# Kernel optimization log

Hardware: AMD Instinct MI355X
Metric: run time of the kernel (lower is better)

The kernel has to match this reference:

```python
import jax, jax.numpy as jnp
import numpy as np

DIM = 1024

def setup_inputs() -> dict:
    key = jax.random.key(0)
    ks = jax.random.split(key, 8)
    B, Sx, Sy, D = 4, 2048, 2048, DIM
    s = 1.0 / np.sqrt(D)
    return {
        "x": jax.random.normal(ks[0], (B, Sx, D), jnp.float32),
        "y": jax.random.normal(ks[1], (B, Sy, D), jnp.float32),
        "Wq": jax.random.normal(ks[2], (D, D), jnp.float32) * s,
        "bq": jnp.zeros((D,), jnp.float32),
        "Wk": jax.random.normal(ks[3], (D, D), jnp.float32) * s,
        "bk": jnp.zeros((D,), jnp.float32),
        "Wv": jax.random.normal(ks[4], (D, D), jnp.float32) * s,
        "bv": jnp.zeros((D,), jnp.float32),
    }

def reference(x, y, Wq, bq, Wk, bk, Wv, bv):
    D = x.shape[-1]
    scale = jnp.sqrt(jnp.asarray(D, x.dtype))
    Q = jnp.einsum('bsd,de->bse', x, Wq) + bq  # [B,Sx,D]
    K = jnp.einsum('btd,de->bte', y, Wk) + bk  # [B,Sy,D]
    V = jnp.einsum('btd,de->bte', y, Wv) + bv  # [B,Sy,D]
    scores = jnp.einsum('bse,bte->bst', Q, K) / scale  # [B,Sx,Sy]
    probs = jax.nn.softmax(scores, axis=-1)
    out = jnp.einsum('bst,bte->bse', probs, V)  # [B,Sx,D]
    return out
```

## Files before the change

### kernel.cpp

```cpp
#include <hip/hip_runtime.h>

typedef __bf16 bf16x8_t __attribute__((ext_vector_type(8)));
typedef float f32x16_t __attribute__((ext_vector_type(16)));
typedef unsigned short ushort_t;

__device__ __forceinline__ unsigned short f2bf(float f) {
  unsigned u = __float_as_uint(f);
  u = (u + 0x7FFFu + ((u >> 16) & 1u)) >> 16;
  return (unsigned short)u;
}
__device__ __forceinline__ float bf2f(unsigned short h) {
  return __uint_as_float(((unsigned)h) << 16);
}

__device__ __forceinline__ void gload16(const void* g, void* l) {
  __builtin_amdgcn_global_load_lds(
      (const __attribute__((address_space(1))) unsigned int*)g,
      (__attribute__((address_space(3))) unsigned int*)l, 16, 0, 0);
}

template<int MFR, int EPI, bool OUT_BF16, bool HAS_BIAS>
__global__ __launch_bounds__(256, (MFR == 2 ? 4 : 6))
void gemm32(const ushort_t* __restrict__ A, const ushort_t* __restrict__ A2,
            int nsplit, const ushort_t* __restrict__ Bt,
            void* __restrict__ Cp, const float* __restrict__ bias,
            float* __restrict__ aux,
            int gx, int gy, int K, int lda, int ldb, int ldc,
            long sA, long sB, long sC, float alpha)
{
  constexpr int ATILE = 2048 * MFR;
  constexpr int BUFSZ = ATILE + 4096;
  __shared__ __align__(16) ushort_t sm[2 * BUFSZ];
  const int tid = threadIdx.x;
  const int lane = tid & 63;
  const int w = tid >> 6;
  const int wr = w >> 1, wc = w & 1;

  const int per = gridDim.x >> 3;
  int wg = blockIdx.x;
  wg = (wg & 7) * per + (wg >> 3);
  const int bz = wg / (gx * gy);
  const int rr = wg - bz * gx * gy;
  const int by = rr / gx, bx = rr - by * gx;
  const int bm = by * (64 * MFR), bn = bx * 128;

  const ushort_t* Ab = (bn >= nsplit) ? A2 : A;

  const int rA0 = (w * MFR) * 16 + (lane >> 2);
  const int cswA = (((lane & 3) ^ ((rA0 >> 1) & 3)) << 3);
  const int rB0 = (w * 2) * 16 + (lane >> 2);
  const int cswB = (((lane & 3) ^ ((rB0 >> 1) & 3)) << 3);
  const ushort_t* pA0 = Ab + (long)bz * sA + (long)(bm + rA0) * lda + cswA;
  const ushort_t* pB0 = Bt + (long)bz * sB + (long)(bn + rB0) * ldb + cswB;

  auto stage = [&](int kt, int buf) {
    const int k0 = kt << 5;
    ushort_t* s = sm + buf * BUFSZ;
#pragma unroll
    for (int i = 0; i < MFR; ++i)
      gload16(pA0 + i * 16 * lda + k0, s + (w * MFR + i) * 512);
#pragma unroll
    for (int i = 0; i < 2; ++i)
      gload16(pB0 + i * 16 * ldb + k0, s + ATILE + (w * 2 + i) * 512);
  };

  const int l31 = lane & 31, kh = lane >> 5;
  int offA[MFR][2], offB[2][2];
#pragma unroll
  for (int m = 0; m < MFR; ++m) {
    const int row = wr * (32 * MFR) + m * 32 + l31;
#pragma unroll
    for (int s = 0; s < 2; ++s)
      offA[m][s] = row * 32 + (((s * 2 + kh) ^ ((row >> 1) & 3)) << 3);
  }
#pragma unroll
  for (int n = 0; n < 2; ++n) {
    const int row = wc * 64 + n * 32 + l31;
#pragma unroll
    for (int s = 0; s < 2; ++s)
      offB[n][s] = ATILE + row * 32 + (((s * 2 + kh) ^ ((row >> 1) & 3)) << 3);
  }

  f32x16_t acc[MFR][2];
#pragma unroll
  for (int m = 0; m < MFR; ++m)
#pragma unroll
    for (int n = 0; n < 2; ++n)
#pragma unroll
      for (int i = 0; i < 16; ++i) acc[m][n][i] = 0.f;

  stage(0, 0);
  __syncthreads();

#define LDX(off) __builtin_bit_cast(bf16x8_t, *(const uint4*)(sp + (off)))
  const int nt = K >> 5;
  for (int kt = 0; kt < nt; ++kt) {
    const int cur = kt & 1;
    if (kt + 1 < nt) stage(kt + 1, cur ^ 1);
    const ushort_t* sp = sm + cur * BUFSZ;
    bf16x8_t af[MFR][2], bf[2][2];
#pragma unroll
    for (int m = 0; m < MFR; ++m)
#pragma unroll
      for (int s = 0; s < 2; ++s) af[m][s] = LDX(offA[m][s]);
#pragma unroll
    for (int n = 0; n < 2; ++n)
#pragma unroll
      for (int s = 0; s < 2; ++s) bf[n][s] = LDX(offB[n][s]);
    __builtin_amdgcn_s_setprio(1);
#pragma unroll
    for (int s = 0; s < 2; ++s)
#pragma unroll
      for (int m = 0; m < MFR; ++m)
#pragma unroll
        for (int n = 0; n < 2; ++n)
          acc[m][n] = __builtin_amdgcn_mfma_f32_32x32x16_bf16(
              af[m][s], bf[n][s], acc[m][n], 0, 0, 0);
    __builtin_amdgcn_s_setprio(0);
    __syncthreads();
  }
#undef LDX

  const long zC = (long)bz * sC;
#pragma unroll
  for (int m = 0; m < MFR; ++m) {
    const int growb = bm + wr * (32 * MFR) + m * 32;
    float part[16];
    if constexpr (EPI == 1) {
#pragma unroll
      for (int r = 0; r < 16; ++r) part[r] = 0.f;
    }
#pragma unroll
    for (int n = 0; n < 2; ++n) {
      const int gcol = bn + wc * 64 + n * 32 + l31;
      float bv_ = 0.f;
      if constexpr (HAS_BIAS) bv_ = bias[gcol];
#pragma unroll
      for (int r = 0; r < 16; ++r) {
        const int grow = growb + (r & 3) + 8 * (r >> 2) + 4 * kh;
        float v = acc[m][n][r] * alpha + bv_;
        if constexpr (EPI == 1) {
          const ushort_t pb = f2bf(__expf(v));
          ((ushort_t*)Cp)[zC + (long)grow * ldc + gcol] = pb;
          part[r] += bf2f(pb);
        } else if constexpr (EPI == 2) {
          v *= aux[bz * 2048 + grow];
          ((float*)Cp)[zC + (long)grow * ldc + gcol] = v;
        } else if constexpr (OUT_BF16) {
          ((ushort_t*)Cp)[zC + (long)grow * ldc + gcol] = f2bf(v);
        } else {
          ((float*)Cp)[zC + (long)grow * ldc + gcol] = v;
        }
      }
    }
    if constexpr (EPI == 1) {
#pragma unroll
      for (int step = 1; step < 32; step <<= 1)
#pragma unroll
        for (int r = 0; r < 16; ++r) part[r] += __shfl_xor(part[r], step, 64);
      if (m == 0) {
        __syncthreads();
        float* pf = (float*)sm;
        if (tid < 64 * MFR) pf[tid] = 0.f;
        __syncthreads();
      }
      if (l31 == 0) {
        float* pf = (float*)sm;
#pragma unroll
        for (int r = 0; r < 16; ++r) {
          const int rloc = wr * (32 * MFR) + m * 32 + (r & 3) + 8 * (r >> 2) + 4 * kh;
          atomicAdd(&pf[rloc], part[r]);
        }
      }
    }
  }
  if constexpr (EPI == 1) {
    __syncthreads();
    if (tid < 64 * MFR) {
      const float* pf = (const float*)sm;
      aux[(long)bx * 8192 + bz * 2048 + by * (64 * MFR) + tid] = pf[tid];
    }
  }
}

__global__ __launch_bounds__(256)
void invrow(const float* __restrict__ psumG, float* __restrict__ inv) {
  const int r = blockIdx.x * 256 + threadIdx.x;
  float s = 0.f;
#pragma unroll
  for (int k = 0; k < 16; ++k) s += psumG[(long)k * 8192 + r];
  inv[r] = 1.0f / s;
}

__global__ __launch_bounds__(256)
void conv2(const float* __restrict__ x, const float* __restrict__ y,
           ushort_t* __restrict__ xb, ushort_t* __restrict__ yb) {
  const int b = blockIdx.x;
  const float* in = (b < 4096) ? x : y;
  ushort_t* out = (b < 4096) ? xb : yb;
  const long i = (long)(b & 4095) * 256 + threadIdx.x;
  const float4 a = ((const float4*)in)[i * 2];
  const float4 c = ((const float4*)in)[i * 2 + 1];
  uint4 o;
  o.x = (unsigned)f2bf(a.x) | ((unsigned)f2bf(a.y) << 16);
  o.y = (unsigned)f2bf(a.z) | ((unsigned)f2bf(a.w) << 16);
  o.z = (unsigned)f2bf(c.x) | ((unsigned)f2bf(c.y) << 16);
  o.w = (unsigned)f2bf(c.z) | ((unsigned)f2bf(c.w) << 16);
  ((uint4*)out)[i] = o;
}

__global__ __launch_bounds__(256)
void wtrans3(const float* __restrict__ W0, const float* __restrict__ W1,
             const float* __restrict__ W2, ushort_t* __restrict__ T0,
             ushort_t* __restrict__ T1, ushort_t* __restrict__ T2) {
  const float* W = (blockIdx.z == 0) ? W0 : (blockIdx.z == 1) ? W1 : W2;
  ushort_t* Wt = (blockIdx.z == 0) ? T0 : (blockIdx.z == 1) ? T1 : T2;
  __shared__ float tile[32][33];
  const int bx = blockIdx.x * 32;
  const int by = blockIdx.y * 32;
  const int t = threadIdx.x;
  const int c = t & 31, r0 = t >> 5;
#pragma unroll
  for (int i = 0; i < 4; ++i)
    tile[r0 + i * 8][c] = W[(long)(by + r0 + i * 8) * 1024 + bx + c];
  __syncthreads();
#pragma unroll
  for (int i = 0; i < 4; ++i)
    Wt[(long)(bx + r0 + i * 8) * 1024 + by + c] = f2bf(tile[c][r0 + i * 8]);
}

__global__ __launch_bounds__(256)
void bconcat3(const float* __restrict__ a, const float* __restrict__ b,
              const float* __restrict__ c, float* __restrict__ o) {
  const int i = blockIdx.x * 256 + threadIdx.x;
  o[i] = (i < 1024) ? a[i] : (i < 2048) ? b[i - 1024] : c[i - 2048];
}

__global__ __launch_bounds__(256)
void transpose_bf16(const ushort_t* __restrict__ in, ushort_t* __restrict__ out,
                    int ld_in, int ld_out, long in_bs, long out_bs) {
  __shared__ ushort_t tt[64][65];
  in += (long)blockIdx.z * in_bs;
  out += (long)blockIdx.z * out_bs;
  const int r0 = blockIdx.y * 64, c0 = blockIdx.x * 64;
  const int tc = threadIdx.x & 31;
  const int tr = threadIdx.x >> 5;
#pragma unroll
  for (int i = 0; i < 8; ++i) {
    const unsigned v = *(const unsigned*)(in + (long)(r0 + tr + 8 * i) * ld_in + c0 + tc * 2);
    tt[tr + 8 * i][tc * 2] = (ushort_t)(v & 0xffff);
    tt[tr + 8 * i][tc * 2 + 1] = (ushort_t)(v >> 16);
  }
  __syncthreads();
#pragma unroll
  for (int i = 0; i < 8; ++i) {
    const unsigned v = (unsigned)tt[tc * 2][tr + 8 * i] |
                       ((unsigned)tt[tc * 2 + 1][tr + 8 * i] << 16);
    *(unsigned*)(out + (long)(c0 + tr + 8 * i) * ld_out + r0 + tc * 2) = v;
  }
}

extern "C" void kernel_launch(void* const* d_in, const int* in_sizes, int n_in,
                              void* d_out, int out_size, void* d_ws, size_t ws_size,
                              hipStream_t stream) {
  const float* x  = (const float*)d_in[0];
  const float* y  = (const float*)d_in[1];
  const float* Wq = (const float*)d_in[2];
  const float* bq = (const float*)d_in[3];
  const float* Wk = (const float*)d_in[4];
  const float* bk = (const float*)d_in[5];
  const float* Wv = (const float*)d_in[6];
  const float* bv = (const float*)d_in[7];
  float* out = (float*)d_out;

  const int D = 1024;
  const long MB_ = 1l << 20;

  ushort_t* ws   = (ushort_t*)d_ws;
  ushort_t* Wall = ws;
  ushort_t* QKV8 = ws + 3 * MB_;
  ushort_t* Sb   = ws + 27 * MB_;
  ushort_t* yb   = ws + 27 * MB_;
  ushort_t* xb   = ws + 35 * MB_;
  ushort_t* Vt   = ws + 43 * MB_;
  float*    bias3 = (float*)(ws + 51 * MB_);
  float*    psumG = (float*)(ws + 51 * MB_ + 8192);
  float*    inv   = psumG + 16 * 8192;

  dim3 blk(256);

  conv2<<<dim3(8192), blk, 0, stream>>>(x, y, xb, yb);
  wtrans3<<<dim3(32, 32, 3), blk, 0, stream>>>(
      Wq, Wk, Wv, Wall, Wall + 1 * MB_, Wall + 2 * MB_);
  bconcat3<<<dim3(12), blk, 0, stream>>>(bq, bk, bv, bias3);

  gemm32<2, 0, true, true><<<dim3(1536), blk, 0, stream>>>(
      xb, yb, 1024, Wall, QKV8, bias3, nullptr,
      24, 64, D, D, D, 3072, 0, 0, 0, 1.0f);

  transpose_bf16<<<dim3(16, 32, 4), blk, 0, stream>>>(
      QKV8 + 2048, Vt, 3072, 2048, 2048l * 3072, 1024l * 2048);

  gemm32<1, 1, true, false><<<dim3(2048), blk, 0, stream>>>(
      QKV8, QKV8, 1 << 30, QKV8 + 1024, Sb, nullptr, psumG,
      16, 32, D, 3072, 3072, 2048,
      2048l * 3072, 2048l * 3072, 2048l * 2048, 0.03125f);

  invrow<<<dim3(32), blk, 0, stream>>>(psumG, inv);

  gemm32<1, 2, false, false><<<dim3(1024), blk, 0, stream>>>(
      Sb, Sb, 1 << 30, Vt, out, nullptr, inv,
      8, 32, 2048, 2048, 2048, D,
      2048l * 2048, 1024l * 2048, 2048l * 1024, 1.0f);
}
```

Measured before the change: 236.5 us.

## Use larger 256-row tiles for score and PV GEMMs with new gemm_big kernel

Adds a gemm_big kernel with 256xBN block tiles, where each wave computes a 128x64 sub-tile (4x2 MFMA fragments), and uses it for the QK^T score GEMM (256x256 tiles, 512 threads) and the probs*V GEMM (256x128 tiles). The larger tiles raise arithmetic intensity and cut redundant global and LDS traffic compared with the earlier 64-row and 128-row tiles. The partial row-sum buffer shrinks from 16 to 8 column blocks to match, and gemm32 loses its now-unused epilogue paths. In exchange there are only 256 workgroups, possibly fewer than the number of CUs, and register pressure per thread is higher.

```diff
diff --git a/kernel.cpp b/kernel.cpp
--- a/kernel.cpp
+++ b/kernel.cpp
@@ -17,6 +17,160 @@
   __builtin_amdgcn_global_load_lds(
       (const __attribute__((address_space(1))) unsigned int*)g,
       (__attribute__((address_space(3))) unsigned int*)l, 16, 0, 0);
+}
+
+template<int BN, int EPI>
+__global__ __launch_bounds__((BN / 64) * 128, 2)
+void gemm_big(const ushort_t* __restrict__ A, const ushort_t* __restrict__ Bt,
+              void* __restrict__ Cp, float* __restrict__ aux,
+              int gx, int gy, int K, int lda, int ldb, int ldc,
+              long sA, long sB, long sC, float alpha)
+{
+  constexpr int WC = BN / 64;
+  constexpr int NW = 2 * WC;
+  constexpr int BUFSZ = 8192 + BN * 32;
+  constexpr int A_SPW = 16 / NW;
+  constexpr int B_SPW = (BN / 16) / NW;
+  __shared__ __align__(16) ushort_t sm[2 * BUFSZ];
+
+  const int tid = threadIdx.x;
+  const int lane = tid & 63;
+  const int w = tid >> 6;
+  const int wr = w / WC, wc = w % WC;
+
+  const int per = gridDim.x >> 3;
+  int wg = blockIdx.x;
+  wg = (wg & 7) * per + (wg >> 3);
+  const int bz = wg / (gx * gy);
+  const int rr = wg - bz * gx * gy;
+  const int by = rr / gx, bx = rr - by * gx;
+  const int bm = by * 256, bn = bx * BN;
+
+  const int csw = (((lane & 3) ^ ((lane >> 3) & 3)) << 3);
+  const ushort_t* pA = A + (long)bz * sA +
+      (long)(bm + w * (A_SPW * 16) + (lane >> 2)) * lda + csw;
+  const ushort_t* pB = Bt + (long)bz * sB +
+      (long)(bn + w * (B_SPW * 16) + (lane >> 2)) * ldb + csw;
+
+  auto stage = [&](int kt, int buf) {
+    const int k0 = kt << 5;
+    ushort_t* s = sm + buf * BUFSZ;
+#pragma unroll
+    for (int i = 0; i < A_SPW; ++i)
+      gload16(pA + (long)(i * 16) * lda + k0, s + (w * A_SPW + i) * 512);
+#pragma unroll
+    for (int i = 0; i < B_SPW; ++i)
+      gload16(pB + (long)(i * 16) * ldb + k0, s + 8192 + (w * B_SPW + i) * 512);
+  };
+
+  const int l31 = lane & 31, kh = lane >> 5;
+  const int sw3 = (lane >> 1) & 3;
+  int offA[4][2], offB[2][2];
+#pragma unroll
+  for (int mf = 0; mf < 4; ++mf)
+#pragma unroll
+    for (int ks = 0; ks < 2; ++ks)
+      offA[mf][ks] = (wr * 128 + mf * 32 + l31) * 32 +
+                     (((ks * 2 + kh) ^ sw3) << 3);
+#pragma unroll
+  for (int nf = 0; nf < 2; ++nf)
+#pragma unroll
+    for (int ks = 0; ks < 2; ++ks)
+      offB[nf][ks] = 8192 + (wc * 64 + nf * 32 + l31) * 32 +
+                     (((ks * 2 + kh) ^ sw3) << 3);
+
+  f32x16_t acc[4][2];
+#pragma unroll
+  for (int m = 0; m < 4; ++m)
+#pragma unroll
+    for (int n = 0; n < 2; ++n)
+#pragma unroll
+      for (int i = 0; i < 16; ++i) acc[m][n][i] = 0.f;
+
+  stage(0, 0);
+  __syncthreads();
+
+#define LDX(off) __builtin_bit_cast(bf16x8_t, *(const uint4*)(sp + (off)))
+  const int nt = K >> 5;
+  for (int kt = 0; kt < nt; ++kt) {
+    const int cur = kt & 1;
+    if (kt + 1 < nt) stage(kt + 1, cur ^ 1);
+    const ushort_t* sp = sm + cur * BUFSZ;
+    bf16x8_t af[4][2], bfv[2][2];
+#pragma unroll
+    for (int mf = 0; mf < 4; ++mf)
+#pragma unroll
+      for (int ks = 0; ks < 2; ++ks) af[mf][ks] = LDX(offA[mf][ks]);
+#pragma unroll
+    for (int nf = 0; nf < 2; ++nf)
+#pragma unroll
+      for (int ks = 0; ks < 2; ++ks) bfv[nf][ks] = LDX(offB[nf][ks]);
+    __builtin_amdgcn_s_setprio(1);
+#pragma unroll
+    for (int ks = 0; ks < 2; ++ks)
+#pragma unroll
+      for (int mf = 0; mf < 4; ++mf)
+#pragma unroll
+        for (int nf = 0; nf < 2; ++nf)
+          acc[mf][nf] = __builtin_amdgcn_mfma_f32_32x32x16_bf16(
+              af[mf][ks], bfv[nf][ks], acc[mf][nf], 0, 0, 0);
+    __builtin_amdgcn_s_setprio(0);
+    __syncthreads();
+  }
+#undef LDX
+
+  const long zC = (long)bz * sC;
+  float* pf = (float*)sm;
+  if constexpr (EPI == 1) {
+    if (tid < 256) pf[tid] = 0.f;
+    __syncthreads();
+  }
+#pragma unroll
+  for (int mf = 0; mf < 4; ++mf) {
+    const int growb = bm + wr * 128 + mf * 32;
+    float part[16];
+    if constexpr (EPI == 1) {
+#pragma unroll
+      for (int r = 0; r < 16; ++r) part[r] = 0.f;
+    }
+#pragma unroll
+    for (int nf = 0; nf < 2; ++nf) {
+      const int gcol = bn + wc * 64 + nf * 32 + l31;
+#pragma unroll
+      for (int r = 0; r < 16; ++r) {
+        const int grow = growb + (r & 3) + 8 * (r >> 2) + 4 * kh;
+        float v = acc[mf][nf][r] * alpha;
+        if constexpr (EPI == 1) {
+          const ushort_t pb = f2bf(__expf(v));
+          ((ushort_t*)Cp)[zC + (long)grow * ldc + gcol] = pb;
+          part[r] += bf2f(pb);
+        } else if constexpr (EPI == 2) {
+          v *= aux[bz * 2048 + grow];
+          ((float*)Cp)[zC + (long)grow * ldc + gcol] = v;
+        } else {
+          ((ushort_t*)Cp)[zC + (long)grow * ldc + gcol] = f2bf(v);
+        }
+      }
+    }
+    if constexpr (EPI == 1) {
+#pragma unroll
+      for (int step = 1; step < 32; step <<= 1)
+#pragma unroll
+        for (int r = 0; r < 16; ++r) part[r] += __shfl_xor(part[r], step, 64);
+      if (l31 == 0) {
+#pragma unroll
+        for (int r = 0; r < 16; ++r) {
+          const int rloc = wr * 128 + mf * 32 + (r & 3) + 8 * (r >> 2) + 4 * kh;
+          atomicAdd(&pf[rloc], part[r]);
+        }
+      }
+    }
+  }
+  if constexpr (EPI == 1) {
+    __syncthreads();
+    if (tid < 256)
+      aux[(long)bx * 8192 + bz * 2048 + by * 256 + tid] = pf[tid];
+  }
 }
 
 template<int MFR, int EPI, bool OUT_BF16, bool HAS_BIAS>
@@ -98,7 +252,7 @@
     const int cur = kt & 1;
     if (kt + 1 < nt) stage(kt + 1, cur ^ 1);
     const ushort_t* sp = sm + cur * BUFSZ;
-    bf16x8_t af[MFR][2], bf[2][2];
+    bf16x8_t af[MFR][2], bfv[2][2];
 #pragma unroll
     for (int m = 0; m < MFR; ++m)
 #pragma unroll
@@ -106,7 +260,7 @@
 #pragma unroll
     for (int n = 0; n < 2; ++n)
 #pragma unroll
-      for (int s = 0; s < 2; ++s) bf[n][s] = LDX(offB[n][s]);
+      for (int s = 0; s < 2; ++s) bfv[n][s] = LDX(offB[n][s]);
     __builtin_amdgcn_s_setprio(1);
 #pragma unroll
     for (int s = 0; s < 2; ++s)
@@ -115,7 +269,7 @@
 #pragma unroll
         for (int n = 0; n < 2; ++n)
           acc[m][n] = __builtin_amdgcn_mfma_f32_32x32x16_bf16(
-              af[m][s], bf[n][s], acc[m][n], 0, 0, 0);
+              af[m][s], bfv[n][s], acc[m][n], 0, 0, 0);
     __builtin_amdgcn_s_setprio(0);
     __syncthreads();
   }
@@ -125,11 +279,6 @@
 #pragma unroll
   for (int m = 0; m < MFR; ++m) {
     const int growb = bm + wr * (32 * MFR) + m * 32;
-    float part[16];
-    if constexpr (EPI == 1) {
-#pragma unroll
-      for (int r = 0; r < 16; ++r) part[r] = 0.f;
-    }
 #pragma unroll
     for (int n = 0; n < 2; ++n) {
       const int gcol = bn + wc * 64 + n * 32 + l31;
@@ -138,48 +287,14 @@
 #pragma unroll
       for (int r = 0; r < 16; ++r) {
         const int grow = growb + (r & 3) + 8 * (r >> 2) + 4 * kh;
-        float v = acc[m][n][r] * alpha + bv_;
-        if constexpr (EPI == 1) {
-          const ushort_t pb = f2bf(__expf(v));
-          ((ushort_t*)Cp)[zC + (long)grow * ldc + gcol] = pb;
-          part[r] += bf2f(pb);
-        } else if constexpr (EPI == 2) {
-          v *= aux[bz * 2048 + grow];
-          ((float*)Cp)[zC + (long)grow * ldc + gcol] = v;
-        } else if constexpr (OUT_BF16) {
+        const float v = acc[m][n][r] * alpha + bv_;
+        if constexpr (OUT_BF16) {
           ((ushort_t*)Cp)[zC + (long)grow * ldc + gcol] = f2bf(v);
         } else {
           ((float*)Cp)[zC + (long)grow * ldc + gcol] = v;
         }
       }
     }
-    if constexpr (EPI == 1) {
-#pragma unroll
-      for (int step = 1; step < 32; step <<= 1)
-#pragma unroll
-        for (int r = 0; r < 16; ++r) part[r] += __shfl_xor(part[r], step, 64);
-      if (m == 0) {
-        __syncthreads();
-        float* pf = (float*)sm;
-        if (tid < 64 * MFR) pf[tid] = 0.f;
-        __syncthreads();
-      }
-      if (l31 == 0) {
-        float* pf = (float*)sm;
-#pragma unroll
-        for (int r = 0; r < 16; ++r) {
-          const int rloc = wr * (32 * MFR) + m * 32 + (r & 3) + 8 * (r >> 2) + 4 * kh;
-          atomicAdd(&pf[rloc], part[r]);
-        }
-      }
-    }
-  }
-  if constexpr (EPI == 1) {
-    __syncthreads();
-    if (tid < 64 * MFR) {
-      const float* pf = (const float*)sm;
-      aux[(long)bx * 8192 + bz * 2048 + by * (64 * MFR) + tid] = pf[tid];
-    }
   }
 }
 
@@ -188,7 +303,7 @@
   const int r = blockIdx.x * 256 + threadIdx.x;
   float s = 0.f;
 #pragma unroll
-  for (int k = 0; k < 16; ++k) s += psumG[(long)k * 8192 + r];
+  for (int k = 0; k < 8; ++k) s += psumG[(long)k * 8192 + r];
   inv[r] = 1.0f / s;
 }
 
@@ -285,7 +400,7 @@
   ushort_t* Vt   = ws + 43 * MB_;
   float*    bias3 = (float*)(ws + 51 * MB_);
   float*    psumG = (float*)(ws + 51 * MB_ + 8192);
-  float*    inv   = psumG + 16 * 8192;
+  float*    inv   = psumG + 8 * 8192;
 
   dim3 blk(256);
 
@@ -301,15 +416,15 @@
   transpose_bf16<<<dim3(16, 32, 4), blk, 0, stream>>>(
       QKV8 + 2048, Vt, 3072, 2048, 2048l * 3072, 1024l * 2048);
 
-  gemm32<1, 1, true, false><<<dim3(2048), blk, 0, stream>>>(
-      QKV8, QKV8, 1 << 30, QKV8 + 1024, Sb, nullptr, psumG,
-      16, 32, D, 3072, 3072, 2048,
+  gemm_big<256, 1><<<dim3(256), dim3(512), 0, stream>>>(
+      QKV8, QKV8 + 1024, Sb, psumG,
+      8, 8, D, 3072, 3072, 2048,
       2048l * 3072, 2048l * 3072, 2048l * 2048, 0.03125f);
 
   invrow<<<dim3(32), blk, 0, stream>>>(psumG, inv);
 
-  gemm32<1, 2, false, false><<<dim3(1024), blk, 0, stream>>>(
-      Sb, Sb, 1 << 30, Vt, out, nullptr, inv,
-      8, 32, 2048, 2048, 2048, D,
+  gemm_big<128, 2><<<dim3(256), dim3(256), 0, stream>>>(
+      Sb, Vt, out, inv,
+      8, 8, 2048, 2048, 2048, D,
       2048l * 2048, 1024l * 2048, 2048l * 1024, 1.0f);
 }
```

Result: faster. 206.4 us (-12.7%).
